# Performance work log

Measured on AMD Instinct MI355X. Metric: run time of the kernel, lower is better.

Reference implementation:

```python
import jax, jax.numpy as jnp
import numpy as np

D_MODEL = 1024
N_HEADS = 16
HEAD_DIM = D_MODEL // N_HEADS


def setup_inputs() -> dict:
    key = jax.random.key(0)
    k1, k2, k3, k4, k5 = jax.random.split(key, 5)
    s = 1.0 / np.sqrt(D_MODEL)
    return {
        "x": jax.random.normal(k1, (2, 2048, D_MODEL), dtype=jnp.float32),
        "w_qkv": jax.random.normal(k2, (D_MODEL, 3 * D_MODEL), dtype=jnp.float32) * s,
        "b_qkv": jax.random.normal(k3, (3 * D_MODEL,), dtype=jnp.float32) * 0.02,
        "w_proj": jax.random.normal(k4, (D_MODEL, D_MODEL), dtype=jnp.float32) * s,
        "b_proj": jax.random.normal(k5, (D_MODEL,), dtype=jnp.float32) * 0.02,
    }


def reference(x, w_qkv, b_qkv, w_proj, b_proj):
    B, S, D = x.shape
    H, Hd = N_HEADS, HEAD_DIM
    qkv = x @ w_qkv + b_qkv                       # [B,S,3D]
    q, k, v = jnp.split(qkv, 3, axis=-1)
    # split heads -> [B,H,S,Hd]
    q = q.reshape(B, S, H, Hd).transpose(0, 2, 1, 3)
    k = k.reshape(B, S, H, Hd).transpose(0, 2, 1, 3)
    v = v.reshape(B, S, H, Hd).transpose(0, 2, 1, 3)
    scale = 1.0 / jnp.sqrt(jnp.asarray(Hd, dtype=x.dtype))
    scores = jnp.einsum("bhqd,bhkd->bhqk", q, k) * scale  # [B,H,S,S]
    causal = jnp.tril(jnp.ones((S, S), dtype=bool))
    scores = jnp.where(causal, scores, jnp.asarray(-jnp.inf, dtype=scores.dtype))
    attn = jax.nn.softmax(scores, axis=-1)
    out = jnp.einsum("bhqk,bhkd->bhqd", attn, v)  # [B,H,S,Hd]
    out = out.transpose(0, 2, 1, 3).reshape(B, S, D)
    return out @ w_proj + b_proj
```

## Files before the change

kernel.cpp:

```cpp
#include <hip/hip_runtime.h>


typedef float f32x4 __attribute__((ext_vector_type(4)));
typedef float f32x16 __attribute__((ext_vector_type(16)));
typedef short bf16x8 __attribute__((ext_vector_type(8)));

#if __has_builtin(__builtin_amdgcn_exp2f)
#define EXP2(x) __builtin_amdgcn_exp2f(x)
#else
#define EXP2(x) exp2f(x)
#endif

__device__ __forceinline__ unsigned short f2bf(float f) {
  union { float f; unsigned u; } v; v.f = f;
  unsigned u = v.u + 0x7fffu + ((v.u >> 16) & 1u);
  return (unsigned short)(u >> 16);
}

__device__ __forceinline__ void async_load16(const void* g, void* lds) {
  __builtin_amdgcn_global_load_lds(
      (const __attribute__((address_space(1))) void*)g,
      (__attribute__((address_space(3))) void*)lds, 16, 0, 0);
}

__global__ void f32_to_bf16_kernel(const float* __restrict__ in,
                                   unsigned short* __restrict__ out, int n) {
  int i = (blockIdx.x * 256 + threadIdx.x) * 4;
  if (i < n) {
    float4 f = *(const float4*)(in + i);
    ushort4 o;
    o.x = f2bf(f.x); o.y = f2bf(f.y); o.z = f2bf(f.z); o.w = f2bf(f.w);
    *(ushort4*)(out + i) = o;
  }
}

__global__ void transpose_f32_bf16_kernel(const float* __restrict__ in,
                                          unsigned short* __restrict__ out,
                                          int K, int N) {
  __shared__ float tile[32][33];
  int n0 = blockIdx.x * 32, k0 = blockIdx.y * 32;
  int tx = threadIdx.x, ty = threadIdx.y;
#pragma unroll
  for (int i = ty; i < 32; i += 8)
    tile[i][tx] = in[(size_t)(k0 + i) * N + (n0 + tx)];
  __syncthreads();
#pragma unroll
  for (int i = ty; i < 32; i += 8)
    out[(size_t)(n0 + i) * K + (k0 + tx)] = f2bf(tile[tx][i]);
}

template <int MI, int NI>
__device__ __forceinline__ void gemm_mainloop(
    const unsigned short* __restrict__ A,
    const unsigned short* __restrict__ BT,
    int K, int mBlk, int nBlk,
    unsigned short* As, unsigned short* Bs,
    f32x4 (&acc)[MI][NI], int lane, int wave)
{
  const int l16 = lane & 15, quad = lane >> 4;
  const int mW = (wave >> 1) * MI * 16;
  const int nW = (wave & 1) * NI * 16;
  constexpr int AROWS = 2 * MI * 16;
  constexpr int BROWS = 2 * NI * 16;
  constexpr int AINST = AROWS / 64;
  constexpr int BINST = BROWS / 64;
  const int rl = lane >> 2;
  const int cl = (lane & 3) * 8;

  for (int k0 = 0; k0 < K; k0 += 32) {
    __syncthreads();
#pragma unroll
    for (int t = 0; t < AINST; ++t) {
      const int rbase = wave * (AROWS / 4) + t * 16;
      async_load16(A + (size_t)(mBlk + rbase + rl) * K + k0 + cl, &As[rbase * 32]);
    }
#pragma unroll
    for (int t = 0; t < BINST; ++t) {
      const int rbase = wave * (BROWS / 4) + t * 16;
      async_load16(BT + (size_t)(nBlk + rbase + rl) * K + k0 + cl, &Bs[rbase * 32]);
    }
    __syncthreads();

    bf16x8 af[MI], bf[NI];
#pragma unroll
    for (int i = 0; i < MI; ++i)
      af[i] = *(const bf16x8*)&As[(mW + i * 16 + l16) * 32 + quad * 8];
#pragma unroll
    for (int j = 0; j < NI; ++j)
      bf[j] = *(const bf16x8*)&Bs[(nW + j * 16 + l16) * 32 + quad * 8];
#pragma unroll
    for (int i = 0; i < MI; ++i)
#pragma unroll
      for (int j = 0; j < NI; ++j)
        acc[i][j] = __builtin_amdgcn_mfma_f32_16x16x32_bf16(af[i], bf[j], acc[i][j], 0, 0, 0);
  }
}

__global__ __launch_bounds__(256) void qkv_gemm_kernel(
    const unsigned short* __restrict__ A,
    const unsigned short* __restrict__ WT,
    const float* __restrict__ bias,
    unsigned short* __restrict__ QKV)
{
  __shared__ unsigned short As[128 * 32];
  __shared__ unsigned short Bs[128 * 32];
  const int lane = threadIdx.x & 63;
  const int wave = threadIdx.x >> 6;
  const int l16 = lane & 15, quad = lane >> 4;

  f32x4 acc[4][4];
  const f32x4 z4 = {0.f, 0.f, 0.f, 0.f};
#pragma unroll
  for (int i = 0; i < 4; ++i)
#pragma unroll
    for (int j = 0; j < 4; ++j) acc[i][j] = z4;

  gemm_mainloop<4, 4>(A, WT, 1024, blockIdx.x * 128, blockIdx.y * 128,
                      As, Bs, acc, lane, wave);

  const int m0 = blockIdx.x * 128 + (wave >> 1) * 64;
  const int n0 = blockIdx.y * 128 + (wave & 1) * 64;
  const int whichW = n0 >> 10;
  const int bb = m0 >> 11;
  const int sBase = (m0 & 2047);
  const size_t planeE = (size_t)2 * 16 * 2048 * 64;

  if (whichW == 2) {
    unsigned short* Vb = QKV + 2 * planeE;
#pragma unroll
    for (int j = 0; j < 4; ++j) {
      const int rem = (n0 & 1023) + j * 16 + l16;
      const int hh = rem >> 6, hd = rem & 63;
      const float bv = bias[n0 + j * 16 + l16];
      unsigned short* col = Vb + (((size_t)bb * 16 + hh) * 64 + hd) * 2048;
#pragma unroll
      for (int i = 0; i < 4; ++i) {
        unsigned short pk[4];
#pragma unroll
        for (int r = 0; r < 4; ++r) pk[r] = f2bf(acc[i][j][r] + bv);
        *(ushort4*)&col[sBase + i * 16 + quad * 4] = *(ushort4*)pk;
      }
    }
  } else {
    const float scale = (whichW == 0) ? 0.18033688011112042f : 1.0f;
#pragma unroll
    for (int j = 0; j < 4; ++j) {
      const int n = n0 + j * 16 + l16;
      const float bv = bias[n];
      const int rem = n & 1023;
      const int hh = rem >> 6, hd = rem & 63;
      unsigned short* pl = QKV + (size_t)whichW * planeE +
                           (((size_t)bb * 16 + hh) * 2048) * 64 + hd;
#pragma unroll
      for (int r = 0; r < 4; ++r) {
        const int s = sBase + (quad * 4 + r);
#pragma unroll
        for (int i = 0; i < 4; ++i)
          pl[(size_t)(s + i * 16) * 64] = f2bf((acc[i][j][r] + bv) * scale);
      }
    }
  }
}

__global__ __launch_bounds__(256, 2) void attn_kernel(
    const unsigned short* __restrict__ QKV,
    unsigned short* __restrict__ AO)
{
  __shared__ __align__(16) unsigned short Ks[3 * 64 * 64];
  __shared__ __align__(16) unsigned short Vs[3 * 64 * 64];
  const int lane = threadIdx.x & 63;
  const int wave = threadIdx.x >> 6;
  const int l31 = lane & 31;
  const int hi  = lane >> 5;

  const int lin  = blockIdx.x;
  const int xcd  = lin & 7;
  const int slot = lin >> 3;
  const int col  = xcd * 4 + (slot >> 4);
  const int b = col >> 4, h = col & 15;
  const int qg = (slot < 32) ? (slot & 15) : (15 - (slot & 15));
  const int qw = qg * 128 + wave * 32;

  const size_t planeE = (size_t)2 * 16 * 2048 * 64;
  const size_t bhS = ((size_t)b * 16 + h) * (size_t)(2048 * 64);
  const unsigned short* Q   = QKV + bhS;
  const unsigned short* Kg  = QKV + planeE + bhS;
  const unsigned short* VTg = QKV + 2 * planeE + bhS;

  bf16x8 qf_[4];
#pragma unroll
  for (int t = 0; t < 4; ++t)
    qf_[t] = *(const bf16x8*)(Q + (size_t)(qw + l31) * 64 + t * 16 + hi * 8);

  bf16x8 onesf;
#pragma unroll
  for (int i = 0; i < 8; ++i) onesf[i] = (short)0x3F80;

  f32x16 O[2], Osum;
#pragma unroll
  for (int r = 0; r < 16; ++r) { O[0][r] = 0.f; O[1][r] = 0.f; Osum[r] = 0.f; }

  const int tbase = (wave & 1) * 4;
  const bool doV = wave >= 2;

  auto stage = [&](int tileIdx, int bufIdx) {
    const int kt = tileIdx * 64;
    unsigned short* Kb = Ks + bufIdx * 4096;
    unsigned short* Vb = Vs + bufIdx * 4096;
#pragma unroll
    for (int i = 0; i < 4; ++i) {
      const int t = tbase + i;
      const int s = t * 64 + lane;
      const int row = s >> 3;
      const int c = (s & 7) ^ (row & 7);
      if (doV)
        async_load16(VTg + (size_t)row * 2048 + kt + c * 8, Vb + t * 512);
      else
        async_load16(Kg + (size_t)(kt + row) * 64 + c * 8, Kb + t * 512);
    }
  };

  const int nt = qg * 2 + 2;
  stage(0, 0);
  stage(1, 1);
  for (int ti = 0; ti < nt; ++ti) {
    asm volatile("s_waitcnt vmcnt(4)\n\ts_barrier" ::: "memory");
    const int tn = (ti + 2 < nt) ? ti + 2 : nt - 1;
    stage(tn, (ti + 2) % 3);
    const int kt = ti * 64;
    const unsigned short* Kb = Ks + (ti % 3) * 4096;
    const unsigned short* Vb = Vs + (ti % 3) * 4096;

    if (kt <= qw + 31) {
      const bool dmask = (kt + 63 > qw);
#pragma unroll
      for (int kg = 0; kg < 2; ++kg) {
        const int krow = kg * 32 + l31;
        const int ks7 = krow & 7;
        bf16x8 ka[4];
#pragma unroll
        for (int t = 0; t < 4; ++t)
          ka[t] = *(const bf16x8*)&Kb[(krow * 8 + ((t * 2 + hi) ^ ks7)) * 8];

        f32x16 sc;
#pragma unroll
        for (int r = 0; r < 16; ++r) sc[r] = 0.f;
        __builtin_amdgcn_s_setprio(1);
#pragma unroll
        for (int t = 0; t < 4; ++t)
          sc = __builtin_amdgcn_mfma_f32_32x32x16_bf16(ka[t], qf_[t], sc, 0, 0, 0);
        __builtin_amdgcn_s_setprio(0);

        float p[16];
#pragma unroll
        for (int r = 0; r < 16; ++r) {
          float v = sc[r];
          if (dmask) {
            const int key = kt + kg * 32 + (r & 3) + 8 * (r >> 2) + 4 * hi;
            if (key > qw + l31) v = -INFINITY;
          }
          p[r] = EXP2(v);
        }
        unsigned c8[8];
#pragma unroll
        for (int i = 0; i < 8; ++i)
          asm("v_cvt_pk_bf16_f32 %0, %1, %2"
              : "=v"(c8[i]) : "v"(p[2 * i]), "v"(p[2 * i + 1]));

#pragma unroll
        for (int half = 0; half < 2; ++half) {
          unsigned a0 = c8[4 * half + 0], a1 = c8[4 * half + 1];
          unsigned a2 = c8[4 * half + 2], a3 = c8[4 * half + 3];
          asm("v_permlane32_swap_b32 %0, %1" : "+v"(a0), "+v"(a2));
          asm("v_permlane32_swap_b32 %0, %1" : "+v"(a1), "+v"(a3));
          union { unsigned u[4]; bf16x8 v; } pa;
          pa.u[0] = a0; pa.u[1] = a1; pa.u[2] = a2; pa.u[3] = a3;
          const int kc = kg * 2 + half;

          __builtin_amdgcn_s_setprio(1);
          Osum = __builtin_amdgcn_mfma_f32_32x32x16_bf16(pa.v, onesf, Osum, 0, 0, 0);
#pragma unroll
          for (int g = 0; g < 2; ++g) {
            const int vrow = g * 32 + l31;
            bf16x8 vb = *(const bf16x8*)&Vb[(vrow * 8 + ((kc * 2 + hi) ^ (vrow & 7))) * 8];
            O[g] = __builtin_amdgcn_mfma_f32_32x32x16_bf16(pa.v, vb, O[g], 0, 0, 0);
          }
          __builtin_amdgcn_s_setprio(0);
        }
      }
    }
  }

  unsigned short* base = AO + ((size_t)b * 2048 + qw) * 1024 + h * 64 + l31;
#pragma unroll
  for (int r = 0; r < 16; ++r) {
    const float inv = 1.0f / Osum[r];
    const int row = (r & 3) + 8 * (r >> 2) + 4 * hi;
#pragma unroll
    for (int g = 0; g < 2; ++g)
      base[(size_t)row * 1024 + g * 32] = f2bf(O[g][r] * inv);
  }
}

__global__ __launch_bounds__(256) void proj_gemm_kernel(
    const unsigned short* __restrict__ A,
    const unsigned short* __restrict__ WT,
    const float* __restrict__ bias,
    float* __restrict__ out)
{
  __shared__ unsigned short As[64 * 32];
  __shared__ unsigned short Bs[128 * 32];
  const int lane = threadIdx.x & 63;
  const int wave = threadIdx.x >> 6;
  const int l16 = lane & 15, quad = lane >> 4;

  f32x4 acc[2][4];
  const f32x4 z4 = {0.f, 0.f, 0.f, 0.f};
#pragma unroll
  for (int i = 0; i < 2; ++i)
#pragma unroll
    for (int j = 0; j < 4; ++j) acc[i][j] = z4;

  gemm_mainloop<2, 4>(A, WT, 1024, blockIdx.x * 64, blockIdx.y * 128,
                      As, Bs, acc, lane, wave);

  const int m0 = blockIdx.x * 64 + (wave >> 1) * 32;
  const int n0 = blockIdx.y * 128 + (wave & 1) * 64;
#pragma unroll
  for (int i = 0; i < 2; ++i) {
#pragma unroll
    for (int j = 0; j < 4; ++j) {
      const int n = n0 + j * 16 + l16;
      const float bv = bias[n];
#pragma unroll
      for (int r = 0; r < 4; ++r) {
        const int m = m0 + i * 16 + quad * 4 + r;
        out[(size_t)m * 1024 + n] = acc[i][j][r] + bv;
      }
    }
  }
}

extern "C" void kernel_launch(void* const* d_in, const int* in_sizes, int n_in,
                              void* d_out, int out_size, void* d_ws, size_t ws_size,
                              hipStream_t stream) {
  const float* x      = (const float*)d_in[0];
  const float* w_qkv  = (const float*)d_in[1];
  const float* b_qkv  = (const float*)d_in[2];
  const float* w_proj = (const float*)d_in[3];
  const float* b_proj = (const float*)d_in[4];
  float* out = (float*)d_out;

  unsigned short* Xb  = (unsigned short*)d_ws;
  unsigned short* WTq = Xb + (size_t)4096 * 1024;
  unsigned short* WTp = WTq + (size_t)3072 * 1024;
  unsigned short* QKV = WTp + (size_t)1024 * 1024;
  unsigned short* AO  = QKV + (size_t)3 * 4096 * 1024;

  f32_to_bf16_kernel<<<4096, 256, 0, stream>>>(x, Xb, 4096 * 1024);
  transpose_f32_bf16_kernel<<<dim3(96, 32), dim3(32, 8), 0, stream>>>(w_qkv, WTq, 1024, 3072);
  transpose_f32_bf16_kernel<<<dim3(32, 32), dim3(32, 8), 0, stream>>>(w_proj, WTp, 1024, 1024);
  qkv_gemm_kernel<<<dim3(32, 24), 256, 0, stream>>>(Xb, WTq, b_qkv, QKV);
  attn_kernel<<<512, 256, 0, stream>>>(QKV, AO);
  proj_gemm_kernel<<<dim3(64, 8), 256, 0, stream>>>(AO, WTp, b_proj, out);
}
```

Before: 201.5 us.

## Triple-buffer GEMM mainloop with async prefetch and XOR-swizzled LDS layout

Restructures the shared GEMM mainloop used by the QKV and projection kernels into a three-stage ring buffer. Global-to-LDS async loads for tile t+2 are issued while tile t is consumed, and a single waitcnt plus barrier replaces the two syncthreads per iteration. It also adds an XOR swizzle on the 16-byte column groups to reduce LDS bank conflicts, and raises wave priority around the MFMA block. LDS use triples per block, which may reduce occupancy, and the tail iterations re-stage the last tile redundantly.

```diff
diff --git a/kernel.cpp b/kernel.cpp
--- a/kernel.cpp
+++ b/kernel.cpp
@@ -64,36 +64,61 @@
   constexpr int BROWS = 2 * NI * 16;
   constexpr int AINST = AROWS / 64;
   constexpr int BINST = BROWS / 64;
+  constexpr int LOADS = AINST + BINST;
+  constexpr int ABUF = AROWS * 32;
+  constexpr int BBUF = BROWS * 32;
   const int rl = lane >> 2;
-  const int cl = (lane & 3) * 8;
-
-  for (int k0 = 0; k0 < K; k0 += 32) {
-    __syncthreads();
-#pragma unroll
-    for (int t = 0; t < AINST; ++t) {
-      const int rbase = wave * (AROWS / 4) + t * 16;
-      async_load16(A + (size_t)(mBlk + rbase + rl) * K + k0 + cl, &As[rbase * 32]);
-    }
-#pragma unroll
-    for (int t = 0; t < BINST; ++t) {
-      const int rbase = wave * (BROWS / 4) + t * 16;
-      async_load16(BT + (size_t)(nBlk + rbase + rl) * K + k0 + cl, &Bs[rbase * 32]);
-    }
-    __syncthreads();
-
+  const int cl = lane & 3;
+  const int NT = K / 32;
+
+  auto stage = [&](int t, int buf) {
+#pragma unroll
+    for (int i = 0; i < AINST; ++i) {
+      const int rbase = wave * (AROWS / 4) + i * 16;
+      const int row = rbase + rl;
+      const int cg = cl ^ ((row >> 1) & 3);
+      async_load16(A + (size_t)(mBlk + row) * K + t * 32 + cg * 8,
+                   &As[buf * ABUF + rbase * 32]);
+    }
+#pragma unroll
+    for (int i = 0; i < BINST; ++i) {
+      const int rbase = wave * (BROWS / 4) + i * 16;
+      const int row = rbase + rl;
+      const int cg = cl ^ ((row >> 1) & 3);
+      async_load16(BT + (size_t)(nBlk + row) * K + t * 32 + cg * 8,
+                   &Bs[buf * BBUF + rbase * 32]);
+    }
+  };
+
+  stage(0, 0);
+  stage(1, 1);
+  for (int t = 0; t < NT; ++t) {
+    asm volatile("s_waitcnt vmcnt(%0)\n\ts_barrier" :: "n"(LOADS) : "memory");
+    const int tn = (t + 2 < NT) ? t + 2 : NT - 1;
+    stage(tn, (t + 2) % 3);
+
+    const unsigned short* Ab = As + (t % 3) * ABUF;
+    const unsigned short* Bb = Bs + (t % 3) * BBUF;
     bf16x8 af[MI], bf[NI];
 #pragma unroll
-    for (int i = 0; i < MI; ++i)
-      af[i] = *(const bf16x8*)&As[(mW + i * 16 + l16) * 32 + quad * 8];
-#pragma unroll
-    for (int j = 0; j < NI; ++j)
-      bf[j] = *(const bf16x8*)&Bs[(nW + j * 16 + l16) * 32 + quad * 8];
+    for (int i = 0; i < MI; ++i) {
+      const int row = mW + i * 16 + l16;
+      af[i] = *(const bf16x8*)&Ab[row * 32 + (quad ^ ((row >> 1) & 3)) * 8];
+    }
+#pragma unroll
+    for (int j = 0; j < NI; ++j) {
+      const int row = nW + j * 16 + l16;
+      bf[j] = *(const bf16x8*)&Bb[row * 32 + (quad ^ ((row >> 1) & 3)) * 8];
+    }
+    __builtin_amdgcn_s_setprio(1);
 #pragma unroll
     for (int i = 0; i < MI; ++i)
 #pragma unroll
       for (int j = 0; j < NI; ++j)
         acc[i][j] = __builtin_amdgcn_mfma_f32_16x16x32_bf16(af[i], bf[j], acc[i][j], 0, 0, 0);
-  }
+    __builtin_amdgcn_s_setprio(0);
+  }
+  asm volatile("s_waitcnt vmcnt(0)" ::: "memory");
 }
 
 __global__ __launch_bounds__(256) void qkv_gemm_kernel(
@@ -102,8 +127,8 @@
     const float* __restrict__ bias,
     unsigned short* __restrict__ QKV)
 {
-  __shared__ unsigned short As[128 * 32];
-  __shared__ unsigned short Bs[128 * 32];
+  __shared__ unsigned short As[3 * 128 * 32];
+  __shared__ unsigned short Bs[3 * 128 * 32];
   const int lane = threadIdx.x & 63;
   const int wave = threadIdx.x >> 6;
   const int l16 = lane & 15, quad = lane >> 4;
@@ -308,8 +333,8 @@
     const float* __restrict__ bias,
     float* __restrict__ out)
 {
-  __shared__ unsigned short As[64 * 32];
-  __shared__ unsigned short Bs[128 * 32];
+  __shared__ unsigned short As[3 * 64 * 32];
+  __shared__ unsigned short Bs[3 * 128 * 32];
   const int lane = threadIdx.x & 63;
   const int wave = threadIdx.x >> 6;
   const int l16 = lane & 15, quad = lane >> 4;
```

Result: slower. 208.1 us (+3.3%).

## Rewrite QKV GEMM with 256x256 tiles, double-buffered async LDS pipeline

Applied to the files above, without the earlier changes.

Replaces the generic 128x128 QKV GEMM mainloop with a dedicated 512-thread kernel that computes 256x256 output tiles. It double-buffers K-chunks of 64 in LDS using async global-to-LDS loads interleaved with MFMA phases, and uses an XOR swizzle to avoid LDS bank conflicts. It also adds a block-index swizzle for L2 locality and s_setprio around the MFMA bursts. The goal is to hide global load latency and raise MFMA utilisation, at the cost of larger LDS and register use and only 192 blocks, which may leave some CUs idle.

```diff
diff --git a/kernel.cpp b/kernel.cpp
--- a/kernel.cpp
+++ b/kernel.cpp
@@ -96,30 +96,122 @@
   }
 }
 
-__global__ __launch_bounds__(256) void qkv_gemm_kernel(
+__global__ __launch_bounds__(512, 2) void qkv_gemm_kernel(
     const unsigned short* __restrict__ A,
     const unsigned short* __restrict__ WT,
     const float* __restrict__ bias,
     unsigned short* __restrict__ QKV)
 {
-  __shared__ unsigned short As[128 * 32];
-  __shared__ unsigned short Bs[128 * 32];
+  __shared__ __align__(16) unsigned short Al[2][2][256][32];
+  __shared__ __align__(16) unsigned short Bl[2][2][256][32];
   const int lane = threadIdx.x & 63;
   const int wave = threadIdx.x >> 6;
   const int l16 = lane & 15, quad = lane >> 4;
-
-  f32x4 acc[4][4];
+  const int wm = wave >> 2, wn = wave & 3;
+
+  const int bid = blockIdx.x;
+  const int swz = (bid & 7) * 24 + (bid >> 3);
+  const int bx = swz & 15, by = swz >> 4;
+  const int mBlk = bx * 256, nBlk = by * 256;
+
+  const int srow = wave * 32 + (lane >> 2);
+  const int scol = lane & 3;
+
+  auto stage = [&](const unsigned short* __restrict__ G, int gRow0,
+                   unsigned short (*L)[32], int kOff) {
+#pragma unroll
+    for (int i = 0; i < 2; ++i) {
+      const int row = srow + i * 16;
+      const int c = scol ^ ((row >> 1) & 3);
+      async_load16(G + (size_t)(gRow0 + row) * 1024 + kOff + c * 8,
+                   &L[wave * 32 + i * 16][0]);
+    }
+  };
+
+  auto rdA = [&](int buf, int kc, int mi) -> bf16x8 {
+    const int r = wm * 128 + mi * 16 + l16;
+    return *(const bf16x8*)&Al[buf][kc][r][(quad ^ ((r >> 1) & 3)) * 8];
+  };
+  auto rdB = [&](int buf, int kc, int n) -> bf16x8 {
+    const int r = wn * 64 + n * 16 + l16;
+    return *(const bf16x8*)&Bl[buf][kc][r][(quad ^ ((r >> 1) & 3)) * 8];
+  };
+
+  f32x4 acc[8][4];
   const f32x4 z4 = {0.f, 0.f, 0.f, 0.f};
 #pragma unroll
-  for (int i = 0; i < 4; ++i)
+  for (int i = 0; i < 8; ++i)
 #pragma unroll
     for (int j = 0; j < 4; ++j) acc[i][j] = z4;
 
-  gemm_mainloop<4, 4>(A, WT, 1024, blockIdx.x * 128, blockIdx.y * 128,
-                      As, Bs, acc, lane, wave);
-
-  const int m0 = blockIdx.x * 128 + (wave >> 1) * 64;
-  const int n0 = blockIdx.y * 128 + (wave & 1) * 64;
+  stage(A, mBlk, Al[0][0], 0);
+  stage(WT, nBlk, Bl[0][0], 0);
+  stage(A, mBlk, Al[0][1], 32);
+  stage(WT, nBlk, Bl[0][1], 32);
+  asm volatile("s_waitcnt vmcnt(4)\n\ts_barrier" ::: "memory");
+
+  for (int t = 0; t < 16; ++t) {
+    const int cur = t & 1, nxt = cur ^ 1;
+    const int tn = (t + 1 < 16) ? t + 1 : 15;
+    const int kO = tn * 64;
+    bf16x8 bf0[4], bf1[4], af[4];
+
+    stage(A, mBlk, Al[nxt][0], kO);
+#pragma unroll
+    for (int n = 0; n < 4; ++n) bf0[n] = rdB(cur, 0, n);
+#pragma unroll
+    for (int mi = 0; mi < 4; ++mi) af[mi] = rdA(cur, 0, mi);
+    __builtin_amdgcn_s_setprio(1);
+#pragma unroll
+    for (int mi = 0; mi < 4; ++mi)
+#pragma unroll
+      for (int n = 0; n < 4; ++n)
+        acc[mi][n] = __builtin_amdgcn_mfma_f32_16x16x32_bf16(af[mi], bf0[n], acc[mi][n], 0, 0, 0);
+    __builtin_amdgcn_s_setprio(0);
+    asm volatile("s_waitcnt vmcnt(2)\n\ts_barrier" ::: "memory");
+
+    stage(WT, nBlk, Bl[nxt][0], kO);
+#pragma unroll
+    for (int n = 0; n < 4; ++n) bf1[n] = rdB(cur, 1, n);
+#pragma unroll
+    for (int mi = 0; mi < 4; ++mi) af[mi] = rdA(cur, 1, mi);
+    __builtin_amdgcn_s_setprio(1);
+#pragma unroll
+    for (int mi = 0; mi < 4; ++mi)
+#pragma unroll
+      for (int n = 0; n < 4; ++n)
+        acc[mi][n] = __builtin_amdgcn_mfma_f32_16x16x32_bf16(af[mi], bf1[n], acc[mi][n], 0, 0, 0);
+    __builtin_amdgcn_s_setprio(0);
+    asm volatile("s_barrier" ::: "memory");
+
+    stage(A, mBlk, Al[nxt][1], kO + 32);
+#pragma unroll
+    for (int mi = 0; mi < 4; ++mi) af[mi] = rdA(cur, 0, mi + 4);
+    __builtin_amdgcn_s_setprio(1);
+#pragma unroll
+    for (int mi = 0; mi < 4; ++mi)
+#pragma unroll
+      for (int n = 0; n < 4; ++n)
+        acc[mi + 4][n] = __builtin_amdgcn_mfma_f32_16x16x32_bf16(af[mi], bf0[n], acc[mi + 4][n], 0, 0, 0);
+    __builtin_amdgcn_s_setprio(0);
+    asm volatile("s_barrier" ::: "memory");
+
+    stage(WT, nBlk, Bl[nxt][1], kO + 32);
+#pragma unroll
+    for (int mi = 0; mi < 4; ++mi) af[mi] = rdA(cur, 1, mi + 4);
+    __builtin_amdgcn_s_setprio(1);
+#pragma unroll
+    for (int mi = 0; mi < 4; ++mi)
+#pragma unroll
+      for (int n = 0; n < 4; ++n)
+        acc[mi + 4][n] = __builtin_amdgcn_mfma_f32_16x16x32_bf16(af[mi], bf1[n], acc[mi + 4][n], 0, 0, 0);
+    __builtin_amdgcn_s_setprio(0);
+    asm volatile("s_waitcnt vmcnt(4)\n\ts_barrier" ::: "memory");
+  }
+  asm volatile("s_waitcnt vmcnt(0)" ::: "memory");
+
+  const int m0 = mBlk + wm * 128;
+  const int n0 = nBlk + wn * 64;
   const int whichW = n0 >> 10;
   const int bb = m0 >> 11;
   const int sBase = (m0 & 2047);
@@ -134,7 +226,7 @@
       const float bv = bias[n0 + j * 16 + l16];
       unsigned short* col = Vb + (((size_t)bb * 16 + hh) * 64 + hd) * 2048;
 #pragma unroll
-      for (int i = 0; i < 4; ++i) {
+      for (int i = 0; i < 8; ++i) {
         unsigned short pk[4];
 #pragma unroll
         for (int r = 0; r < 4; ++r) pk[r] = f2bf(acc[i][j][r] + bv);
@@ -155,7 +247,7 @@
       for (int r = 0; r < 4; ++r) {
         const int s = sBase + (quad * 4 + r);
 #pragma unroll
-        for (int i = 0; i < 4; ++i)
+        for (int i = 0; i < 8; ++i)
           pl[(size_t)(s + i * 16) * 64] = f2bf((acc[i][j][r] + bv) * scale);
       }
     }
@@ -360,7 +452,7 @@
   f32_to_bf16_kernel<<<4096, 256, 0, stream>>>(x, Xb, 4096 * 1024);
   transpose_f32_bf16_kernel<<<dim3(96, 32), dim3(32, 8), 0, stream>>>(w_qkv, WTq, 1024, 3072);
   transpose_f32_bf16_kernel<<<dim3(32, 32), dim3(32, 8), 0, stream>>>(w_proj, WTp, 1024, 1024);
-  qkv_gemm_kernel<<<dim3(32, 24), 256, 0, stream>>>(Xb, WTq, b_qkv, QKV);
+  qkv_gemm_kernel<<<192, 512, 0, stream>>>(Xb, WTq, b_qkv, QKV);
   attn_kernel<<<512, 256, 0, stream>>>(QKV, AO);
   proj_gemm_kernel<<<dim3(64, 8), 256, 0, stream>>>(AO, WTp, b_proj, out);
 }
```

After: 205.0 us. Within noise of the previous version (+1.7%).
